# Optimization experiments

Hardware: AMD Instinct MI355X
Metric: run time of the kernel (lower is better)

Reference implementation:

```python
import jax, jax.numpy as jnp
import numpy as np

N = 50000   # nodes
E = 1600000 # edges
D = 128     # input_dim
H = 128     # hidden_dim
O = 128     # output_dim
G = 64      # graphs in batch
EPS = 1e-5  # batchnorm eps


def setup_inputs() -> dict:
    key = jax.random.key(0)
    ks = jax.random.split(key, 20)
    x = jax.random.normal(ks[0], (N, D), jnp.float32)
    edge_index = jax.random.randint(ks[1], (2, E), 0, N, dtype=jnp.int32)
    batch = jnp.sort(jax.random.randint(ks[2], (N,), 0, G, dtype=jnp.int32))

    def lin(k, fi, fo):
        return jax.random.normal(k, (fi, fo), jnp.float32) / np.float32(np.sqrt(fi))

    return {
        "x": x, "edge_index": edge_index, "batch": batch,
        "W1": lin(ks[3], D, H), "b1": jnp.zeros((H,), jnp.float32),
        "W2": lin(ks[4], H, H), "b2": jnp.zeros((H,), jnp.float32),
        "W3": lin(ks[5], H, O), "b3": jnp.zeros((O,), jnp.float32),
        "g1": 1.0 + 0.1 * jax.random.normal(ks[6], (H,), jnp.float32),
        "be1": 0.1 * jax.random.normal(ks[7], (H,), jnp.float32),
        "rm1": 0.1 * jax.random.normal(ks[8], (H,), jnp.float32),
        "rv1": 0.5 + jax.random.uniform(ks[9], (H,), jnp.float32),
        "g2": 1.0 + 0.1 * jax.random.normal(ks[10], (H,), jnp.float32),
        "be2": 0.1 * jax.random.normal(ks[11], (H,), jnp.float32),
        "rm2": 0.1 * jax.random.normal(ks[12], (H,), jnp.float32),
        "rv2": 0.5 + jax.random.uniform(ks[13], (H,), jnp.float32),
    }


def _gcn_layer(h, W, b, row, col, norm):
    # h: [N, Fin] -> [N, Fout]; GCN: A_hat @ (h W) + b with sym-normalized A_hat
    h = h @ W
    msg = h[row] * norm[:, None]                      # [E+N, Fout] gather
    out = jax.ops.segment_sum(msg, col, num_segments=N)
    return out + b


def _bn_eval(h, g, be, rm, rv):
    return (h - rm) * jax.lax.rsqrt(rv + EPS) * g + be


def reference(x, edge_index, batch, W1, b1, W2, b2, W3, b3,
              g1, be1, rm1, rv1, g2, be2, rm2, rv2):
    # add self loops (PyG GCNConv default)
    loop = jnp.arange(N, dtype=edge_index.dtype)
    row = jnp.concatenate([edge_index[0], loop])
    col = jnp.concatenate([edge_index[1], loop])
    deg = jax.ops.segment_sum(jnp.ones_like(col, jnp.float32), col, num_segments=N)
    dinv = jnp.where(deg > 0, jax.lax.rsqrt(jnp.maximum(deg, 1.0)), 0.0)
    norm = dinv[row] * dinv[col]                       # [E+N]

    h = _gcn_layer(x, W1, b1, row, col, norm)
    h = jax.nn.relu(_bn_eval(h, g1, be1, rm1, rv1))    # dropout is identity (eval)
    h = _gcn_layer(h, W2, b2, row, col, norm)
    h = jax.nn.relu(_bn_eval(h, g2, be2, rm2, rv2))
    h = _gcn_layer(h, W3, b3, row, col, norm)
    # global_add_pool by graph id
    return jax.ops.segment_sum(h, batch, num_segments=G)  # [G, O]
```

## Files before the change

kernel.cpp:

```cpp
#include <hip/hip_runtime.h>
#include <hip/hip_bf16.h>

#define NN 50000
#define NE 1600000
#define DIM 128
#define NG 64
#define EPSV 1e-5f
#define NCHUNK 49
#define UNROLL 8
#define RUN 4
#define NXCD 8
#define SHARD_COLS (NN / NXCD)
#define FILL_CHUNKS 256

typedef __attribute__((ext_vector_type(8))) __bf16 bf16x8;
typedef __attribute__((ext_vector_type(2))) __bf16 bf16x2;
typedef __attribute__((ext_vector_type(16))) float f32x16;


__global__ void count_kernel(const int* __restrict__ ecol, int* __restrict__ cnt) {
    int e = blockIdx.x * 256 + threadIdx.x;
    if (e < NE) atomicAdd(&cnt[ecol[e]], 1);
}

__global__ void scan_chunk(const int* __restrict__ cnt, int* __restrict__ excl,
                           int* __restrict__ csum) {
    __shared__ int lds[256];
    int t = threadIdx.x;
    int base = blockIdx.x * 1024 + t * 4;
    int v0 = (base + 0 < NN) ? cnt[base + 0] : 0;
    int v1 = (base + 1 < NN) ? cnt[base + 1] : 0;
    int v2 = (base + 2 < NN) ? cnt[base + 2] : 0;
    int v3 = (base + 3 < NN) ? cnt[base + 3] : 0;
    int s = v0 + v1 + v2 + v3;
    lds[t] = s;
    __syncthreads();
    for (int off = 1; off < 256; off <<= 1) {
        int x = (t >= off) ? lds[t - off] : 0;
        __syncthreads();
        lds[t] += x;
        __syncthreads();
    }
    int run = lds[t] - s;
    if (t == 255) csum[blockIdx.x] = lds[t];
    if (base + 0 < NN) excl[base + 0] = run; run += v0;
    if (base + 1 < NN) excl[base + 1] = run; run += v1;
    if (base + 2 < NN) excl[base + 2] = run; run += v2;
    if (base + 3 < NN) excl[base + 3] = run;
}

__global__ void scan_tail(const int* __restrict__ csum, int* __restrict__ coff, int nch) {
    int l = threadIdx.x;
    int v = (l < nch) ? csum[l] : 0;
    int s = v;
    for (int o = 1; o < 64; o <<= 1) {
        int x = __shfl_up(s, o);
        if (l >= o) s += x;
    }
    if (l < nch) coff[l] = s - v;
}

__global__ void fixup_kernel(int* __restrict__ row_ptr, const int* __restrict__ coff,
                             const int* __restrict__ cnt, float* __restrict__ dinv,
                             int* __restrict__ cursor) {
    int n = blockIdx.x * 256 + threadIdx.x;
    if (n < NN) {
        int rp = row_ptr[n] + coff[n >> 10];
        row_ptr[n] = rp;
        cursor[n] = rp;
        dinv[n] = rsqrtf((float)(cnt[n] + 1));
    }
    if (n == 0) row_ptr[NN] = NE;
}

__global__ void fill_kernel(const int* __restrict__ erow, const int* __restrict__ ecol,
                            int* __restrict__ cursor, int* __restrict__ esrc) {
    const int shard = blockIdx.x & (NXCD - 1);
    const int chunk = blockIdx.x >> 3;
    const int lo = shard * SHARD_COLS;
    const int hi = lo + SHARD_COLS;
    for (int e = chunk * 256 + threadIdx.x; e < NE; e += FILL_CHUNKS * 256) {
        const int c = ecol[e];
        if (c >= lo && c < hi) {
            int pos = atomicAdd(&cursor[c], 1);
            esrc[pos] = erow[e];
        }
    }
}

__global__ void bn_prep_kernel(const float* __restrict__ b1, const float* __restrict__ g1,
                               const float* __restrict__ be1, const float* __restrict__ rm1,
                               const float* __restrict__ rv1,
                               const float* __restrict__ b2, const float* __restrict__ g2,
                               const float* __restrict__ be2, const float* __restrict__ rm2,
                               const float* __restrict__ rv2,
                               float* __restrict__ sc1, float* __restrict__ sh1,
                               float* __restrict__ sc2, float* __restrict__ sh2) {
    int c = threadIdx.x;
    if (c < DIM) {
        float s1 = g1[c] * rsqrtf(rv1[c] + EPSV);
        sc1[c] = s1;
        sh1[c] = (b1[c] - rm1[c]) * s1 + be1[c];
        float s2 = g2[c] * rsqrtf(rv2[c] + EPSV);
        sc2[c] = s2;
        sh2[c] = (b2[c] - rm2[c]) * s2 + be2[c];
    }
}


__device__ __forceinline__ bf16x8 load8(const float* p) {
    float4 lo = ((const float4*)p)[0], hi = ((const float4*)p)[1];
    bf16x8 a;
    a[0] = (__bf16)lo.x; a[1] = (__bf16)lo.y; a[2] = (__bf16)lo.z; a[3] = (__bf16)lo.w;
    a[4] = (__bf16)hi.x; a[5] = (__bf16)hi.y; a[6] = (__bf16)hi.z; a[7] = (__bf16)hi.w;
    return a;
}
__device__ __forceinline__ bf16x8 load8(const __bf16* p) {
    return *(const bf16x8*)p;
}

template <typename T>
__global__ void __launch_bounds__(256) matmul_kernel(const T* __restrict__ h,
                                                     const float* __restrict__ W,
                                                     const float* __restrict__ dinv,
                                                     __bf16* __restrict__ t) {
    const int wave = threadIdx.x >> 6;
    const int lane = threadIdx.x & 63;
    const int col = wave * 32 + (lane & 31);
    const int khalf = (lane >> 5) * 8;

    bf16x8 b[8];
#pragma unroll
    for (int kc = 0; kc < 8; kc++) {
#pragma unroll
        for (int j = 0; j < 8; j++) {
            b[kc][j] = (__bf16)W[(kc * 16 + khalf + j) * DIM + col];
        }
    }

    const int ntiles = (NN + 31) / 32;
    for (int tile = blockIdx.x; tile < ntiles; tile += gridDim.x) {
        const int arow = tile * 32 + (lane & 31);
        const int arow_c = (arow < NN) ? arow : (NN - 1);
        f32x16 acc = {};
#pragma unroll
        for (int kc = 0; kc < 8; kc++) {
            bf16x8 a = load8(h + (size_t)arow_c * DIM + kc * 16 + khalf);
            acc = __builtin_amdgcn_mfma_f32_32x32x16_bf16(a, b[kc], acc, 0, 0, 0);
        }
#pragma unroll
        for (int r = 0; r < 16; r++) {
            int orow = tile * 32 + (r & 3) + 8 * (r >> 2) + 4 * (lane >> 5);
            if (orow < NN) t[(size_t)orow * DIM + col] = (__bf16)(acc[r] * dinv[orow]);
        }
    }
}


__device__ __forceinline__ void gather_core(
    const unsigned int* __restrict__ t32, const int* __restrict__ esrc,
    int beg, int end, int lane, float& ax, float& ay) {
    for (int e = beg; e < end; e += UNROLL) {
        int   s[UNROLL];
        float w[UNROLL];
        unsigned int u[UNROLL];
#pragma unroll
        for (int i = 0; i < UNROLL; i++) {
            const bool ok = (e + i) < end;
            s[i] = esrc[ok ? (e + i) : beg];
            w[i] = ok ? 1.f : 0.f;
        }
#pragma unroll
        for (int i = 0; i < UNROLL; i++) u[i] = t32[(size_t)s[i] * 64 + lane];
#pragma unroll
        for (int i = 0; i < UNROLL; i++) {
            ax = fmaf(__uint_as_float(u[i] << 16), w[i], ax);
            ay = fmaf(__uint_as_float(u[i] & 0xffff0000u), w[i], ay);
        }
    }
}

__global__ void __launch_bounds__(256) gather_bn_kernel(
    const unsigned int* __restrict__ t32, const int* __restrict__ row_ptr,
    const int* __restrict__ esrc, const float* __restrict__ dinv,
    const float* __restrict__ scale, const float* __restrict__ shift,
    __bf16* __restrict__ out) {
    const int lane = threadIdx.x & 63;
    const int n = __builtin_amdgcn_readfirstlane(blockIdx.x * 4 + (threadIdx.x >> 6));
    if (n >= NN) return;
    float ax = 0.f, ay = 0.f;
    const int beg = row_ptr[n], end = row_ptr[n + 1];
    gather_core(t32, esrc, beg, end, lane, ax, ay);
    {
        const unsigned int u = t32[(size_t)n * 64 + lane];
        ax += __uint_as_float(u << 16);
        ay += __uint_as_float(u & 0xffff0000u);
    }
    const float dv = dinv[n];
    const int c0 = lane * 2, c1 = c0 + 1;
    ax = fmaxf(fmaf(ax, dv * scale[c0], shift[c0]), 0.f);
    ay = fmaxf(fmaf(ay, dv * scale[c1], shift[c1]), 0.f);
    bf16x2 o; o[0] = (__bf16)ax; o[1] = (__bf16)ay;
    *(bf16x2*)(out + (size_t)n * DIM + c0) = o;
}


__global__ void __launch_bounds__(256) gather_pool_kernel(
    const unsigned int* __restrict__ t32, const int* __restrict__ row_ptr,
    const int* __restrict__ esrc, const float* __restrict__ dinv,
    const float* __restrict__ bias, const int* __restrict__ batch,
    float* __restrict__ out) {
    const int lane = threadIdx.x & 63;
    const int wid = __builtin_amdgcn_readfirstlane(blockIdx.x * 4 + (threadIdx.x >> 6));
    const int n0 = wid * RUN;
    if (n0 >= NN) return;
    const int n1 = (n0 + RUN < NN) ? n0 + RUN : NN;
    const int c0 = lane * 2, c1 = c0 + 1;
    const float bx = bias[c0], by = bias[c1];
    float rx = 0.f, ry = 0.f;
    int g = batch[n0];
    for (int n = n0; n < n1; ++n) {
        float ax = 0.f, ay = 0.f;
        const int beg = row_ptr[n], end = row_ptr[n + 1];
        gather_core(t32, esrc, beg, end, lane, ax, ay);
        {
            const unsigned int u = t32[(size_t)n * 64 + lane];
            ax += __uint_as_float(u << 16);
            ay += __uint_as_float(u & 0xffff0000u);
        }
        const float dv = dinv[n];
        const int gn = batch[n];
        if (gn != g) {
            atomicAdd(out + (size_t)g * DIM + c0, rx);
            atomicAdd(out + (size_t)g * DIM + c1, ry);
            rx = 0.f; ry = 0.f; g = gn;
        }
        rx += fmaf(ax, dv, bx);
        ry += fmaf(ay, dv, by);
    }
    atomicAdd(out + (size_t)g * DIM + c0, rx);
    atomicAdd(out + (size_t)g * DIM + c1, ry);
}


extern "C" void kernel_launch(void* const* d_in, const int* in_sizes, int n_in,
                              void* d_out, int out_size, void* d_ws, size_t ws_size,
                              hipStream_t stream) {
    const float* x    = (const float*)d_in[0];
    const int*   ei   = (const int*)d_in[1];
    const int*   batch= (const int*)d_in[2];
    const float* W1 = (const float*)d_in[3];
    const float* b1 = (const float*)d_in[4];
    const float* W2 = (const float*)d_in[5];
    const float* b2 = (const float*)d_in[6];
    const float* W3 = (const float*)d_in[7];
    const float* b3 = (const float*)d_in[8];
    const float* g1 = (const float*)d_in[9];
    const float* be1= (const float*)d_in[10];
    const float* rm1= (const float*)d_in[11];
    const float* rv1= (const float*)d_in[12];
    const float* g2 = (const float*)d_in[13];
    const float* be2= (const float*)d_in[14];
    const float* rm2= (const float*)d_in[15];
    const float* rv2= (const float*)d_in[16];
    const int* erow = ei;
    const int* ecol = ei + NE;

    char* ws = (char*)d_ws;
    size_t off = 0;
    auto alloc = [&](size_t bytes) -> void* {
        void* p = ws + off;
        off = (off + bytes + 255) & ~(size_t)255;
        return p;
    };
    int*    cnt     = (int*)alloc(NN * sizeof(int));
    int*    row_ptr = (int*)alloc((NN + 1) * sizeof(int));
    int*    cursor  = (int*)alloc(NN * sizeof(int));
    int*    csum    = (int*)alloc(64 * sizeof(int));
    int*    coff    = (int*)alloc(64 * sizeof(int));
    float*  dinv    = (float*)alloc(NN * sizeof(float));
    int*    esrc    = (int*)alloc(NE * sizeof(int));
    __bf16* tbuf    = (__bf16*)alloc((size_t)NN * DIM * sizeof(__bf16));
    __bf16* hbuf    = (__bf16*)alloc((size_t)NN * DIM * sizeof(__bf16));
    float*  sc1     = (float*)alloc(DIM * sizeof(float));
    float*  sh1     = (float*)alloc(DIM * sizeof(float));
    float*  sc2     = (float*)alloc(DIM * sizeof(float));
    float*  sh2     = (float*)alloc(DIM * sizeof(float));

    hipMemsetAsync(cnt, 0, NN * sizeof(int), stream);
    hipMemsetAsync(d_out, 0, NG * DIM * sizeof(float), stream);

    bn_prep_kernel<<<1, 128, 0, stream>>>(b1, g1, be1, rm1, rv1,
                                          b2, g2, be2, rm2, rv2,
                                          sc1, sh1, sc2, sh2);
    count_kernel<<<(NE + 255) / 256, 256, 0, stream>>>(ecol, cnt);
    scan_chunk<<<NCHUNK, 256, 0, stream>>>(cnt, row_ptr, csum);
    scan_tail<<<1, 64, 0, stream>>>(csum, coff, NCHUNK);
    fixup_kernel<<<(NN + 255) / 256, 256, 0, stream>>>(row_ptr, coff, cnt, dinv, cursor);
    fill_kernel<<<NXCD * FILL_CHUNKS, 256, 0, stream>>>(erow, ecol, cursor, esrc);

    const unsigned int* t32 = (const unsigned int*)tbuf;
    const int nblk = (NN + 3) / 4;
    const int nwaves_pool = (NN + RUN - 1) / RUN;
    const int nblk_pool = (nwaves_pool + 3) / 4;

    matmul_kernel<float><<<512, 256, 0, stream>>>(x, W1, dinv, tbuf);
    gather_bn_kernel<<<nblk, 256, 0, stream>>>(t32, row_ptr, esrc, dinv,
                                               sc1, sh1, hbuf);
    matmul_kernel<__bf16><<<512, 256, 0, stream>>>(hbuf, W2, dinv, tbuf);
    gather_bn_kernel<<<nblk, 256, 0, stream>>>(t32, row_ptr, esrc, dinv,
                                               sc2, sh2, hbuf);
    matmul_kernel<__bf16><<<512, 256, 0, stream>>>(hbuf, W3, dinv, tbuf);
    gather_pool_kernel<<<nblk_pool, 256, 0, stream>>>(t32, row_ptr, esrc, dinv,
                                                      b3, batch, (float*)d_out);
}
```

Baseline: 401.9 us.

## Slice feature matrices into 16-column planes so gathers stay cache-resident per slice

Stores the transformed node features in a column-sliced layout (8 planes of 16 bf16 columns each) and splits every gather kernel into 8 slice blocks. Each wave then processes 8 edges at once with 8 lanes per edge, followed by a shuffle reduction. The aim is to shrink the per-slice working set of random gathers so it fits in the L2 or Infinity Cache, and to add memory-level parallelism across edges. It also adds nontemporal loads on edge arrays. The cost is 8x more launches of index reads (esrc and row_ptr are re-read once per slice), cross-lane reductions, and 32-byte rows that may underuse the cache line.

```diff
diff --git a/kernel.cpp b/kernel.cpp
--- a/kernel.cpp
+++ b/kernel.cpp
@@ -7,11 +7,11 @@
 #define NG 64
 #define EPSV 1e-5f
 #define NCHUNK 49
-#define UNROLL 8
 #define RUN 4
 #define NXCD 8
 #define SHARD_COLS (NN / NXCD)
 #define FILL_CHUNKS 256
+#define SLICES 8
 
 typedef __attribute__((ext_vector_type(8))) __bf16 bf16x8;
 typedef __attribute__((ext_vector_type(2))) __bf16 bf16x2;
@@ -20,7 +20,7 @@
 
 __global__ void count_kernel(const int* __restrict__ ecol, int* __restrict__ cnt) {
     int e = blockIdx.x * 256 + threadIdx.x;
-    if (e < NE) atomicAdd(&cnt[ecol[e]], 1);
+    if (e < NE) atomicAdd(&cnt[__builtin_nontemporal_load(&ecol[e])], 1);
 }
 
 __global__ void scan_chunk(const int* __restrict__ cnt, int* __restrict__ excl,
@@ -80,10 +80,10 @@
     const int lo = shard * SHARD_COLS;
     const int hi = lo + SHARD_COLS;
     for (int e = chunk * 256 + threadIdx.x; e < NE; e += FILL_CHUNKS * 256) {
-        const int c = ecol[e];
+        const int c = __builtin_nontemporal_load(&ecol[e]);
         if (c >= lo && c < hi) {
             int pos = atomicAdd(&cursor[c], 1);
-            esrc[pos] = erow[e];
+            esrc[pos] = __builtin_nontemporal_load(&erow[e]);
         }
     }
 }
@@ -119,7 +119,7 @@
     return *(const bf16x8*)p;
 }
 
-template <typename T>
+template <typename T, bool SLICED_IN>
 __global__ void __launch_bounds__(256) matmul_kernel(const T* __restrict__ h,
                                                      const float* __restrict__ W,
                                                      const float* __restrict__ dinv,
@@ -145,101 +145,124 @@
         f32x16 acc = {};
 #pragma unroll
         for (int kc = 0; kc < 8; kc++) {
-            bf16x8 a = load8(h + (size_t)arow_c * DIM + kc * 16 + khalf);
+            const T* p = SLICED_IN
+                ? h + (size_t)kc * NN * 16 + (size_t)arow_c * 16 + khalf
+                : h + (size_t)arow_c * DIM + kc * 16 + khalf;
+            bf16x8 a = load8(p);
             acc = __builtin_amdgcn_mfma_f32_32x32x16_bf16(a, b[kc], acc, 0, 0, 0);
         }
+        const size_t sbase = (size_t)(col >> 4) * NN * 16 + (col & 15);
 #pragma unroll
         for (int r = 0; r < 16; r++) {
             int orow = tile * 32 + (r & 3) + 8 * (r >> 2) + 4 * (lane >> 5);
-            if (orow < NN) t[(size_t)orow * DIM + col] = (__bf16)(acc[r] * dinv[orow]);
-        }
-    }
-}
-
-
-__device__ __forceinline__ void gather_core(
-    const unsigned int* __restrict__ t32, const int* __restrict__ esrc,
-    int beg, int end, int lane, float& ax, float& ay) {
-    for (int e = beg; e < end; e += UNROLL) {
-        int   s[UNROLL];
-        float w[UNROLL];
-        unsigned int u[UNROLL];
-#pragma unroll
-        for (int i = 0; i < UNROLL; i++) {
-            const bool ok = (e + i) < end;
-            s[i] = esrc[ok ? (e + i) : beg];
-            w[i] = ok ? 1.f : 0.f;
-        }
-#pragma unroll
-        for (int i = 0; i < UNROLL; i++) u[i] = t32[(size_t)s[i] * 64 + lane];
-#pragma unroll
-        for (int i = 0; i < UNROLL; i++) {
-            ax = fmaf(__uint_as_float(u[i] << 16), w[i], ax);
-            ay = fmaf(__uint_as_float(u[i] & 0xffff0000u), w[i], ay);
-        }
+            if (orow < NN) t[sbase + (size_t)orow * 16] = (__bf16)(acc[r] * dinv[orow]);
+        }
+    }
+}
+
+
+__device__ __forceinline__ float lo16(unsigned u) { return __uint_as_float(u << 16); }
+__device__ __forceinline__ float hi16(unsigned u) { return __uint_as_float(u & 0xffff0000u); }
+
+__device__ __forceinline__ void gather_slice(
+    const unsigned* __restrict__ ts, const int* __restrict__ esrc,
+    int beg, int end, int grp, int sub, float& ax, float& ay) {
+    if (beg >= end) return;
+    int sA; float wA; unsigned uA;
+    {
+        const int ee = beg + grp;
+        const bool ok = ee < end;
+        sA = __builtin_nontemporal_load(&esrc[ok ? ee : beg]);
+        wA = ok ? 1.f : 0.f;
+        uA = ts[(size_t)sA * 8 + sub];
+    }
+    for (int e = beg; e < end;) {
+        const int e2 = e + 8;
+        int sB; float wB; unsigned uB;
+        if (e2 < end) {
+            const int ee = e2 + grp;
+            const bool ok = ee < end;
+            sB = __builtin_nontemporal_load(&esrc[ok ? ee : beg]);
+            wB = ok ? 1.f : 0.f;
+            uB = ts[(size_t)sB * 8 + sub];
+        }
+        ax = fmaf(lo16(uA), wA, ax);
+        ay = fmaf(hi16(uA), wA, ay);
+        e = e2;
+        sA = sB; wA = wB; uA = uB;
     }
 }
 
 __global__ void __launch_bounds__(256) gather_bn_kernel(
-    const unsigned int* __restrict__ t32, const int* __restrict__ row_ptr,
+    const unsigned* __restrict__ t32, const int* __restrict__ row_ptr,
     const int* __restrict__ esrc, const float* __restrict__ dinv,
     const float* __restrict__ scale, const float* __restrict__ shift,
     __bf16* __restrict__ out) {
+    const int slice = blockIdx.x & (SLICES - 1);
     const int lane = threadIdx.x & 63;
-    const int n = __builtin_amdgcn_readfirstlane(blockIdx.x * 4 + (threadIdx.x >> 6));
+    const int grp = lane >> 3, sub = lane & 7;
+    const int n = __builtin_amdgcn_readfirstlane((blockIdx.x >> 3) * 4 + (threadIdx.x >> 6));
     if (n >= NN) return;
+    const unsigned* ts = t32 + (size_t)slice * NN * 8;
+    const int beg = row_ptr[n], end = row_ptr[n + 1];
     float ax = 0.f, ay = 0.f;
-    const int beg = row_ptr[n], end = row_ptr[n + 1];
-    gather_core(t32, esrc, beg, end, lane, ax, ay);
-    {
-        const unsigned int u = t32[(size_t)n * 64 + lane];
-        ax += __uint_as_float(u << 16);
-        ay += __uint_as_float(u & 0xffff0000u);
-    }
-    const float dv = dinv[n];
-    const int c0 = lane * 2, c1 = c0 + 1;
-    ax = fmaxf(fmaf(ax, dv * scale[c0], shift[c0]), 0.f);
-    ay = fmaxf(fmaf(ay, dv * scale[c1], shift[c1]), 0.f);
-    bf16x2 o; o[0] = (__bf16)ax; o[1] = (__bf16)ay;
-    *(bf16x2*)(out + (size_t)n * DIM + c0) = o;
+    gather_slice(ts, esrc, beg, end, grp, sub, ax, ay);
+    ax += __shfl_xor(ax, 8); ax += __shfl_xor(ax, 16); ax += __shfl_xor(ax, 32);
+    ay += __shfl_xor(ay, 8); ay += __shfl_xor(ay, 16); ay += __shfl_xor(ay, 32);
+    if (lane < 8) {
+        const unsigned u = ts[(size_t)n * 8 + lane];
+        ax += lo16(u); ay += hi16(u);
+        const float dv = dinv[n];
+        const int c0 = slice * 16 + lane * 2;
+        const float vx = fmaxf(fmaf(ax, dv * scale[c0], shift[c0]), 0.f);
+        const float vy = fmaxf(fmaf(ay, dv * scale[c0 + 1], shift[c0 + 1]), 0.f);
+        bf16x2 o; o[0] = (__bf16)vx; o[1] = (__bf16)vy;
+        *(bf16x2*)(out + (size_t)slice * NN * 16 + (size_t)n * 16 + lane * 2) = o;
+    }
 }
 
 
 __global__ void __launch_bounds__(256) gather_pool_kernel(
-    const unsigned int* __restrict__ t32, const int* __restrict__ row_ptr,
+    const unsigned* __restrict__ t32, const int* __restrict__ row_ptr,
     const int* __restrict__ esrc, const float* __restrict__ dinv,
     const float* __restrict__ bias, const int* __restrict__ batch,
     float* __restrict__ out) {
+    const int slice = blockIdx.x & (SLICES - 1);
     const int lane = threadIdx.x & 63;
-    const int wid = __builtin_amdgcn_readfirstlane(blockIdx.x * 4 + (threadIdx.x >> 6));
+    const int grp = lane >> 3, sub = lane & 7;
+    const int wid = __builtin_amdgcn_readfirstlane((blockIdx.x >> 3) * 4 + (threadIdx.x >> 6));
     const int n0 = wid * RUN;
     if (n0 >= NN) return;
-    const int n1 = (n0 + RUN < NN) ? n0 + RUN : NN;
-    const int c0 = lane * 2, c1 = c0 + 1;
-    const float bx = bias[c0], by = bias[c1];
+    const unsigned* ts = t32 + (size_t)slice * NN * 8;
+    const int c0 = slice * 16 + sub * 2;
+    const float bx = bias[c0], by = bias[c0 + 1];
     float rx = 0.f, ry = 0.f;
     int g = batch[n0];
-    for (int n = n0; n < n1; ++n) {
+    for (int j = 0; j < RUN; j++) {
+        const int n = n0 + j;
+        const int beg = row_ptr[n], end = row_ptr[n + 1];
         float ax = 0.f, ay = 0.f;
-        const int beg = row_ptr[n], end = row_ptr[n + 1];
-        gather_core(t32, esrc, beg, end, lane, ax, ay);
-        {
-            const unsigned int u = t32[(size_t)n * 64 + lane];
-            ax += __uint_as_float(u << 16);
-            ay += __uint_as_float(u & 0xffff0000u);
-        }
+        gather_slice(ts, esrc, beg, end, grp, sub, ax, ay);
+        ax += __shfl_xor(ax, 8); ax += __shfl_xor(ax, 16); ax += __shfl_xor(ax, 32);
+        ay += __shfl_xor(ay, 8); ay += __shfl_xor(ay, 16); ay += __shfl_xor(ay, 32);
+        const unsigned u = ts[(size_t)n * 8 + sub];
+        ax += lo16(u); ay += hi16(u);
         const float dv = dinv[n];
         const int gn = batch[n];
         if (gn != g) {
-            atomicAdd(out + (size_t)g * DIM + c0, rx);
-            atomicAdd(out + (size_t)g * DIM + c1, ry);
+            if (lane < 8) {
+                atomicAdd(out + (size_t)g * DIM + c0, rx);
+                atomicAdd(out + (size_t)g * DIM + c0 + 1, ry);
+            }
             rx = 0.f; ry = 0.f; g = gn;
         }
         rx += fmaf(ax, dv, bx);
         ry += fmaf(ay, dv, by);
     }
-    atomicAdd(out + (size_t)g * DIM + c0, rx);
-    atomicAdd(out + (size_t)g * DIM + c1, ry);
+    if (lane < 8) {
+        atomicAdd(out + (size_t)g * DIM + c0, rx);
+        atomicAdd(out + (size_t)g * DIM + c0 + 1, ry);
+    }
 }
 
 
@@ -299,18 +322,17 @@
     fixup_kernel<<<(NN + 255) / 256, 256, 0, stream>>>(row_ptr, coff, cnt, dinv, cursor);
     fill_kernel<<<NXCD * FILL_CHUNKS, 256, 0, stream>>>(erow, ecol, cursor, esrc);
 
-    const unsigned int* t32 = (const unsigned int*)tbuf;
-    const int nblk = (NN + 3) / 4;
-    const int nwaves_pool = (NN + RUN - 1) / RUN;
-    const int nblk_pool = (nwaves_pool + 3) / 4;
-
-    matmul_kernel<float><<<512, 256, 0, stream>>>(x, W1, dinv, tbuf);
-    gather_bn_kernel<<<nblk, 256, 0, stream>>>(t32, row_ptr, esrc, dinv,
-                                               sc1, sh1, hbuf);
-    matmul_kernel<__bf16><<<512, 256, 0, stream>>>(hbuf, W2, dinv, tbuf);
-    gather_bn_kernel<<<nblk, 256, 0, stream>>>(t32, row_ptr, esrc, dinv,
-                                               sc2, sh2, hbuf);
-    matmul_kernel<__bf16><<<512, 256, 0, stream>>>(hbuf, W3, dinv, tbuf);
+    const unsigned* t32 = (const unsigned*)tbuf;
+    const int nblk_bn = SLICES * ((NN + 3) / 4);
+    const int nblk_pool = SLICES * ((NN / RUN + 3) / 4);
+
+    matmul_kernel<float, false><<<512, 256, 0, stream>>>(x, W1, dinv, tbuf);
+    gather_bn_kernel<<<nblk_bn, 256, 0, stream>>>(t32, row_ptr, esrc, dinv,
+                                                  sc1, sh1, hbuf);
+    matmul_kernel<__bf16, true><<<512, 256, 0, stream>>>(hbuf, W2, dinv, tbuf);
+    gather_bn_kernel<<<nblk_bn, 256, 0, stream>>>(t32, row_ptr, esrc, dinv,
+                                                  sc2, sh2, hbuf);
+    matmul_kernel<__bf16, true><<<512, 256, 0, stream>>>(hbuf, W3, dinv, tbuf);
     gather_pool_kernel<<<nblk_pool, 256, 0, stream>>>(t32, row_ptr, esrc, dinv,
                                                       b3, batch, (float*)d_out);
 }
```

Result: slower. 821.4 us (+104.4%).
